# Performance work log

Measured on AMD Instinct MI355X. Metric: run time of the kernel, lower is better.

The kernel has to match this reference:

```python
import jax, jax.numpy as jnp
import numpy as np

B, N, C = 2, 8192, 64      # batch, points, feature channels
M = 2048                    # FPS-sampled centers (num_point)
KS = (16, 32)               # KNN sizes per scale
H, O = 128, 128             # EGNN hidden / output channels
S = len(KS)


def setup_inputs() -> dict:
    key = jax.random.key(0)
    k = jax.random.split(key, 12)
    sc = 0.05
    return {
        "points_xyz": jax.random.normal(k[0], (B, N, 3), jnp.float32),
        "features":   jax.random.normal(k[1], (B, C, N), jnp.float32),
        # edge MLP phi_e: [h_i, h_j, ||x_i-x_j||^2] -> H -> H
        "we1": jax.random.normal(k[2], (S, 2 * C + 1, H)) * sc,
        "be1": jnp.zeros((S, H)),
        "we2": jax.random.normal(k[3], (S, H, H)) * sc,
        "be2": jnp.zeros((S, H)),
        # coord MLP phi_x: H -> 1
        "wx": jax.random.normal(k[4], (S, H, 1)) * sc,
        "bx": jnp.zeros((S, 1)),
        # node MLP phi_h: [h_i, sum_j m_ij] -> H -> O
        "wh1": jax.random.normal(k[5], (S, C + H, H)) * sc,
        "bh1": jnp.zeros((S, H)),
        "wh2": jax.random.normal(k[6], (S, H, O)) * sc,
        "bh2": jnp.zeros((S, O)),
    }


def fps(xyz, m):
    """D-FPS: farthest point sampling by Euclidean distance. xyz (B,N,3) -> idx (B,m) int32."""
    b, n, _ = xyz.shape
    start = jnp.zeros((b,), jnp.int32)
    mind0 = jnp.full((b, n), 1e10, xyz.dtype)

    def step(carry, _):
        mind, last = carry
        lxyz = jnp.take_along_axis(xyz, last[:, None, None], axis=1)  # (B,1,3)
        d = jnp.sum((xyz - lxyz) ** 2, axis=-1)                       # (B,N)
        mind = jnp.minimum(mind, d)
        nxt = jnp.argmax(mind, axis=1).astype(jnp.int32)
        return (mind, nxt), nxt

    (_, _), rest = jax.lax.scan(step, (mind0, start), None, length=m - 1)
    return jnp.concatenate([start[:, None], rest.T], axis=1)  # (B,m)


def _forward(points_xyz, features, we1, be1, we2, be2, wx, bx, wh1, bh1, wh2, bh2):
    idx = fps(points_xyz, M)                                           # (B,M)
    dsamp_xyz = jnp.take_along_axis(points_xyz, idx[:, :, None], axis=1)   # (B,M,3)
    dsamp_feat = jnp.take_along_axis(features, idx[:, None, :], axis=2)    # (B,C,M)
    h_i = dsamp_feat.transpose(0, 2, 1)                                # (B,M,C)

    # pairwise squared distances centers->all points (B,M,N)
    d2 = (jnp.sum(dsamp_xyz ** 2, -1)[:, :, None]
          + jnp.sum(points_xyz ** 2, -1)[:, None, :]
          - 2.0 * jnp.einsum('bmd,bnd->bmn', dsamp_xyz, points_xyz))

    shifted, feats = [], []
    for i, k in enumerate(KS):
        _, nidx = jax.lax.top_k(-d2, k)                                # (B,M,k) KNN indices
        neigh_xyz = jax.vmap(lambda p, ii: p[ii])(points_xyz, nidx)    # (B,M,k,3)
        neigh_feat = jax.vmap(lambda f, ii: f[:, ii])(features, nidx)  # (B,C,M,k)
        h_j = neigh_feat.transpose(0, 2, 3, 1)                         # (B,M,k,C)

        rel = dsamp_xyz[:, :, None, :] - neigh_xyz                     # (B,M,k,3)
        dist2 = jnp.sum(rel * rel, -1, keepdims=True)                  # (B,M,k,1)

        e_in = jnp.concatenate(
            [jnp.broadcast_to(h_i[:, :, None, :], h_j.shape), h_j, dist2], axis=-1)
        m_ij = jax.nn.silu(e_in @ we1[i] + be1[i])
        m_ij = jax.nn.silu(m_ij @ we2[i] + be2[i])                     # (B,M,k,H)

        coef = m_ij @ wx[i] + bx[i]                                    # (B,M,k,1)
        x_shift = dsamp_xyz + jnp.mean(rel * coef, axis=2)             # (B,M,3)

        agg = jnp.sum(m_ij, axis=2)                                    # (B,M,H)
        h_out = jax.nn.silu(jnp.concatenate([h_i, agg], -1) @ wh1[i] + bh1[i]) @ wh2[i] + bh2[i]

        shifted.append(x_shift)
        feats.append(h_out.transpose(0, 2, 1))                         # (B,O,M)

    return (dsamp_xyz,
            jnp.concatenate(shifted, axis=1),    # (B, S*M, 3)
            jnp.concatenate(feats, axis=1),      # (B, S*O, M)
            idx)


def reference(points_xyz, features, we1, be1, we2, be2, wx, bx, wh1, bh1, wh2, bh2):
    return _forward(points_xyz, features, we1, be1, we2, be2, wx, bx, wh1, bh1, wh2, bh2)
```

## Files before the change

### kernel.cpp

```cpp
#include <hip/hip_runtime.h>
#include <stdint.h>
#include <math.h>

#define NPTS  8192
#define NB    2
#define NC    64
#define MCENT 2048
#define HH    128
#define K2NN  32

#define OUT0_OFF 0
#define OUT1_OFF (NB*MCENT*3)
#define OUT2_OFF (OUT1_OFF + NB*2*MCENT*3)
#define OUT3_OFF (OUT2_OFF + NB*2*HH*MCENT)

__device__ __forceinline__ float silu_f(float v){ return v / (1.0f + expf(-v)); }

template<int CTRL>
__device__ __forceinline__ unsigned dppk(unsigned v){
  return (unsigned)__builtin_amdgcn_update_dpp((int)v, (int)v, CTRL, 0xF, 0xF, false);
}
__device__ __forceinline__ unsigned wave_max_u32_sgpr(unsigned v){
  unsigned s;
  s = dppk<0xB1>(v);  v = v > s ? v : s;
  s = dppk<0x4E>(v);  v = v > s ? v : s;
  s = dppk<0x141>(v); v = v > s ? v : s;
  s = dppk<0x140>(v); v = v > s ? v : s;
  s = dppk<0x142>(v); v = v > s ? v : s;
  s = dppk<0x143>(v); v = v > s ? v : s;
  return (unsigned)__builtin_amdgcn_readlane((int)v, 63);
}
__device__ __forceinline__ unsigned wave_min_u32_sgpr(unsigned v){
  unsigned s;
  s = dppk<0xB1>(v);  v = v < s ? v : s;
  s = dppk<0x4E>(v);  v = v < s ? v : s;
  s = dppk<0x141>(v); v = v < s ? v : s;
  s = dppk<0x140>(v); v = v < s ? v : s;
  s = dppk<0x142>(v); v = v < s ? v : s;
  s = dppk<0x143>(v); v = v < s ? v : s;
  return (unsigned)__builtin_amdgcn_readlane((int)v, 63);
}

__device__ __forceinline__ void bar_lds(){
  asm volatile("s_waitcnt lgkmcnt(0)" ::: "memory");
  __builtin_amdgcn_s_barrier();
  __builtin_amdgcn_sched_barrier(0);
}

__global__ __launch_bounds__(1024, 4) void fps_kernel(const float* __restrict__ xyz,
                                                      float* __restrict__ out,
                                                      int* __restrict__ ws_idx){
#pragma clang fp contract(off)
  __shared__ float xs[NPTS], ys[NPTS], zs[NPTS];
  __shared__ unsigned long long warr[2][16];
  const int b    = blockIdx.x;
  const int tid  = threadIdx.x;
  const int lane = tid & 63, wid = tid >> 6;
  const float* P = xyz + (size_t)b * NPTS * 3;

  float x[8], y[8], z[8], mind[8];
  #pragma unroll
  for (int j = 0; j < 8; ++j){
    const int p = tid*8 + j;
    const float px = P[p*3+0], py = P[p*3+1], pz = P[p*3+2];
    x[j] = px; y[j] = py; z[j] = pz; mind[j] = 1e10f;
    xs[p] = px; ys[p] = py; zs[p] = pz;
  }
  float cx = P[0], cy = P[1], cz = P[2];
  if (tid == 0){
    ws_idx[b*MCENT] = 0;
    out[OUT3_OFF + b*MCENT] = 0.0f;
    out[OUT0_OFF + (size_t)(b*MCENT)*3 + 0] = cx;
    out[OUT0_OFF + (size_t)(b*MCENT)*3 + 1] = cy;
    out[OUT0_OFF + (size_t)(b*MCENT)*3 + 2] = cz;
  }
  __syncthreads();

  for (int t = 1; t < MCENT; ++t){
    float bestv = -1.0f; int bestp = tid*8;
    #pragma unroll
    for (int j = 0; j < 8; ++j){
      const float dx = x[j]-cx, dy = y[j]-cy, dz = z[j]-cz;
      const float d  = (dx*dx + dy*dy) + dz*dz;
      const float mn = fminf(mind[j], d);
      mind[j] = mn;
      if (mn > bestv){ bestv = mn; bestp = tid*8 + j; }
    }
    const unsigned vb = __float_as_uint(bestv);
    const unsigned wv = wave_max_u32_sgpr(vb);
    const unsigned long long bal = __ballot(vb == wv);
    const int wl = __ffsll(bal) - 1;
    const int wp = __builtin_amdgcn_readlane(bestp, wl);
    if (lane == 0)
      warr[t & 1][wid] = ((unsigned long long)wv << 32) | (unsigned)(NPTS-1-wp);
    bar_lds();
    unsigned long long kb = warr[t & 1][0];
    #pragma unroll
    for (int w = 1; w < 16; ++w){
      const unsigned long long k2 = warr[t & 1][w];
      if (k2 > kb) kb = k2;
    }
    const int p = NPTS - 1 - (int)(kb & 0xFFFFFFFFULL);
    cx = xs[p]; cy = ys[p]; cz = zs[p];
    if (tid == 0){
      ws_idx[b*MCENT + t] = p;
      out[OUT3_OFF + b*MCENT + t] = (float)p;
      out[OUT0_OFF + (size_t)(b*MCENT + t)*3 + 0] = cx;
      out[OUT0_OFF + (size_t)(b*MCENT + t)*3 + 1] = cy;
      out[OUT0_OFF + (size_t)(b*MCENT + t)*3 + 2] = cz;
    }
  }
}

__global__ __launch_bounds__(256) void knn_kernel(const float* __restrict__ xyz,
                                                  const float* __restrict__ out,
                                                  int* __restrict__ ws_knn){
#pragma clang fp contract(off)
  __shared__ unsigned d2u[NPTS];
  __shared__ unsigned long long warr[2][4];
  const int blk = blockIdx.x;
  const int b = blk / MCENT, m = blk % MCENT;
  const int tid = threadIdx.x;
  const float* P = xyz + (size_t)b*NPTS*3;
  const float cx = out[OUT0_OFF + (size_t)(b*MCENT+m)*3 + 0];
  const float cy = out[OUT0_OFF + (size_t)(b*MCENT+m)*3 + 1];
  const float cz = out[OUT0_OFF + (size_t)(b*MCENT+m)*3 + 2];
  const float cn = (cx*cx + cy*cy) + cz*cz;

  unsigned long long best = ~0ULL, second = ~0ULL;
  #pragma unroll 4
  for (int j = 0; j < NPTS/256; ++j){
    const int p = tid + 256*j;
    const float px = P[p*3+0], py = P[p*3+1], pz = P[p*3+2];
    const float pn = (px*px + py*py) + pz*pz;
    const float e  = (cx*px + cy*py) + cz*pz;
    const float d2 = (cn + pn) - 2.0f*e;
    unsigned u = __float_as_uint(d2);
    u = (u & 0x80000000u) ? ~u : (u | 0x80000000u);
    d2u[p] = u;
    const unsigned long long kk = ((unsigned long long)u << 32) | (unsigned)p;
    if      (kk < best)  { second = best; best = kk; }
    else if (kk < second){ second = kk; }
  }
  __syncthreads();

  for (int it = 0; it < K2NN; ++it){
    const unsigned vb = (unsigned)(best >> 32);
    const unsigned wv = wave_min_u32_sgpr(vb);
    const unsigned long long bal = __ballot(vb == wv);
    unsigned long long k;
    if (__popcll(bal) == 1){
      const int wl = __ffsll(bal) - 1;
      const unsigned lp = (unsigned)__builtin_amdgcn_readlane((int)(unsigned)best, wl);
      k = ((unsigned long long)wv << 32) | lp;
    } else {
      k = best;
      #pragma unroll
      for (int o = 32; o > 0; o >>= 1){
        const unsigned long long k2 = __shfl_xor(k, o);
        if (k2 < k) k = k2;
      }
    }
    if ((tid & 63) == 0) warr[it & 1][tid >> 6] = k;
    __syncthreads();
    unsigned long long kb = warr[it & 1][0];
    #pragma unroll
    for (int w = 1; w < 4; ++w){
      const unsigned long long k2 = warr[it & 1][w];
      if (k2 < kb) kb = k2;
    }
    const unsigned p = (unsigned)kb;
    if (tid == 0) ws_knn[(size_t)blk*K2NN + it] = (int)p;
    if (best == kb){
      d2u[p] = 0xFFFFFFFFu;
      best = second; second = ~0ULL;
      if (best == ~0ULL){
        #pragma unroll 4
        for (int j = 0; j < NPTS/256; ++j){
          const int q = tid + 256*j;
          const unsigned long long kk = ((unsigned long long)d2u[q] << 32) | (unsigned)q;
          if      (kk < best)  { second = best; best = kk; }
          else if (kk < second){ second = kk; }
        }
      }
    }
  }
}

#define S1STR 132

template<int KNB>
__device__ __forceinline__ void egnn_scale(
    int isc, int b, int m, int tid,
    const float* __restrict__ we1, const float* __restrict__ be1,
    const float* __restrict__ we2, const float* __restrict__ be2,
    const float* __restrict__ wxw, const float* __restrict__ bxw,
    const float* __restrict__ wh1, const float* __restrict__ bh1,
    const float* __restrict__ wh2, const float* __restrict__ bh2,
    const float* hi, const float (*hj)[NC], const float (*rel)[3],
    const float* d2s, float (*s1)[S1STR], float (*s2)[S1STR],
    float* coefs, float* aggs, float* t1,
    float cx, float cy, float cz, float* __restrict__ out)
{
  constexpr int KH = KNB/2;
  const int h  = tid & 127;
  const int jg = tid >> 7;
  const int j0 = jg * KH;
  const float* W1 = we1 + (size_t)isc*129*HH;
  const float* W2 = we2 + (size_t)isc*HH*HH;

  float shi = be1[isc*HH + h];
  for (int r = 0; r < NC; ++r) shi += hi[r] * W1[r*HH + h];
  float acc[KH];
  #pragma unroll
  for (int jl = 0; jl < KH; ++jl) acc[jl] = shi;
  for (int r4 = 0; r4 < NC/4; ++r4){
    const float w0 = W1[(NC + 4*r4+0)*HH + h];
    const float w1 = W1[(NC + 4*r4+1)*HH + h];
    const float w2 = W1[(NC + 4*r4+2)*HH + h];
    const float w3 = W1[(NC + 4*r4+3)*HH + h];
    #pragma unroll
    for (int jl = 0; jl < KH; ++jl){
      const float4 v = *(const float4*)&hj[j0+jl][4*r4];
      acc[jl] += v.x*w0; acc[jl] += v.y*w1; acc[jl] += v.z*w2; acc[jl] += v.w*w3;
    }
  }
  {
    const float wd = W1[128*HH + h];
    #pragma unroll
    for (int jl = 0; jl < KH; ++jl)
      s1[j0+jl][h] = silu_f(acc[jl] + d2s[j0+jl]*wd);
  }
  __syncthreads();

  float acc2[KH];
  {
    const float b2 = be2[isc*HH + h];
    #pragma unroll
    for (int jl = 0; jl < KH; ++jl) acc2[jl] = b2;
  }
  for (int r4 = 0; r4 < HH/4; ++r4){
    const float w0 = W2[(4*r4+0)*HH + h];
    const float w1 = W2[(4*r4+1)*HH + h];
    const float w2 = W2[(4*r4+2)*HH + h];
    const float w3 = W2[(4*r4+3)*HH + h];
    #pragma unroll
    for (int jl = 0; jl < KH; ++jl){
      const float4 v = *(const float4*)&s1[j0+jl][4*r4];
      acc2[jl] += v.x*w0; acc2[jl] += v.y*w1; acc2[jl] += v.z*w2; acc2[jl] += v.w*w3;
    }
  }
  #pragma unroll
  for (int jl = 0; jl < KH; ++jl)
    s2[j0+jl][h] = silu_f(acc2[jl]);
  __syncthreads();

  if (tid < HH){
    float a = 0.f;
    #pragma unroll
    for (int j = 0; j < KNB; ++j) a += s2[j][tid];
    aggs[tid] = a;
  } else if (tid < HH + KNB){
    const int j = tid - HH;
    const float* WX = wxw + isc*HH;
    float c = 0.f;
    for (int r = 0; r < HH; ++r) c += s2[j][r]*WX[r];
    coefs[j] = c + bxw[isc];
  }
  __syncthreads();

  if (tid < 3){
    float s = 0.f;
    #pragma unroll
    for (int j = 0; j < KNB; ++j) s += rel[j][tid]*coefs[j];
    const float cc = (tid==0) ? cx : ((tid==1) ? cy : cz);
    out[OUT1_OFF + ((size_t)(b*2 + isc)*MCENT + m)*3 + tid] = cc + s*(1.0f/KNB);
  }

  if (tid < HH){
    const float* WH1 = wh1 + (size_t)isc*(NC+HH)*HH;
    float n = bh1[isc*HH + tid];
    for (int r = 0; r < NC; ++r) n += hi[r]*WH1[r*HH + tid];
    for (int r = 0; r < HH; ++r) n += aggs[r]*WH1[(NC+r)*HH + tid];
    t1[tid] = silu_f(n);
  }
  __syncthreads();

  if (tid < HH){
    const float* WH2 = wh2 + (size_t)isc*HH*HH;
    float v = bh2[isc*HH + tid];
    for (int r = 0; r < HH; ++r) v += t1[r]*WH2[r*HH + tid];
    out[OUT2_OFF + ((size_t)(b*2*HH) + isc*HH + tid)*MCENT + m] = v;
  }
  __syncthreads();
}

__global__ __launch_bounds__(256) void egnn_kernel(
    const float* __restrict__ xyz,  const float* __restrict__ feat,
    const float* __restrict__ we1,  const float* __restrict__ be1,
    const float* __restrict__ we2,  const float* __restrict__ be2,
    const float* __restrict__ wxw,  const float* __restrict__ bxw,
    const float* __restrict__ wh1,  const float* __restrict__ bh1,
    const float* __restrict__ wh2,  const float* __restrict__ bh2,
    const int* __restrict__ ws_idx, const int* __restrict__ ws_knn,
    float* __restrict__ out)
{
  __shared__ __align__(16) float hi[NC];
  __shared__ __align__(16) float hj[K2NN][NC];
  __shared__ float rel[K2NN][3];
  __shared__ float d2s[K2NN];
  __shared__ __align__(16) float s1[K2NN][S1STR];
  __shared__ __align__(16) float s2[K2NN][S1STR];
  __shared__ float coefs[K2NN];
  __shared__ float aggs[HH];
  __shared__ float t1[HH];
  __shared__ int   nidx[K2NN];

  const int blk = blockIdx.x;
  const int b = blk / MCENT, m = blk % MCENT;
  const int tid = threadIdx.x;
  const float* P = xyz + (size_t)b*NPTS*3;
  const float cx = out[OUT0_OFF + (size_t)(b*MCENT+m)*3 + 0];
  const float cy = out[OUT0_OFF + (size_t)(b*MCENT+m)*3 + 1];
  const float cz = out[OUT0_OFF + (size_t)(b*MCENT+m)*3 + 2];

  const int ci = ws_idx[b*MCENT + m];
  if (tid < NC)   hi[tid]   = feat[((size_t)b*NC + tid)*NPTS + ci];
  if (tid < K2NN) nidx[tid] = ws_knn[(size_t)blk*K2NN + tid];
  __syncthreads();

  if (tid < K2NN){
    const int p = nidx[tid];
    const float rx = cx - P[p*3+0];
    const float ry = cy - P[p*3+1];
    const float rz = cz - P[p*3+2];
    rel[tid][0]=rx; rel[tid][1]=ry; rel[tid][2]=rz;
    d2s[tid] = rx*rx + ry*ry + rz*rz;
  }
  {
    const int j  = tid >> 3;
    const int c0 = (tid & 7) * 8;
    const int p  = nidx[j];
    #pragma unroll
    for (int q = 0; q < 8; ++q)
      hj[j][c0+q] = feat[((size_t)b*NC + c0 + q)*NPTS + p];
  }
  __syncthreads();

  egnn_scale<16>(0, b, m, tid, we1, be1, we2, be2, wxw, bxw, wh1, bh1, wh2, bh2,
                 hi, hj, rel, d2s, s1, s2, coefs, aggs, t1, cx, cy, cz, out);
  egnn_scale<32>(1, b, m, tid, we1, be1, we2, be2, wxw, bxw, wh1, bh1, wh2, bh2,
                 hi, hj, rel, d2s, s1, s2, coefs, aggs, t1, cx, cy, cz, out);
}

extern "C" void kernel_launch(void* const* d_in, const int* in_sizes, int n_in,
                              void* d_out, int out_size, void* d_ws, size_t ws_size,
                              hipStream_t stream){
  const float* xyz = (const float*)d_in[0];
  const float* feat= (const float*)d_in[1];
  const float* we1 = (const float*)d_in[2];
  const float* be1 = (const float*)d_in[3];
  const float* we2 = (const float*)d_in[4];
  const float* be2 = (const float*)d_in[5];
  const float* wxw = (const float*)d_in[6];
  const float* bxw = (const float*)d_in[7];
  const float* wh1 = (const float*)d_in[8];
  const float* bh1 = (const float*)d_in[9];
  const float* wh2 = (const float*)d_in[10];
  const float* bh2 = (const float*)d_in[11];
  float* out = (float*)d_out;

  int* ws_idx = (int*)d_ws;
  int* ws_knn = ws_idx + NB*MCENT;

  fps_kernel <<<dim3(NB),        dim3(1024), 0, stream>>>(xyz, out, ws_idx);
  knn_kernel <<<dim3(NB*MCENT),  dim3(256),  0, stream>>>(xyz, out, ws_knn);
  egnn_kernel<<<dim3(NB*MCENT),  dim3(256),  0, stream>>>(xyz, feat,
      we1, be1, we2, be2, wxw, bxw, wh1, bh1, wh2, bh2, ws_idx, ws_knn, out);
}
```

Before: 2.665 ms.

## Fuse KNN into EGNN kernel and shrink FPS block to 256 threads

The KNN selection moves into the EGNN kernel. Its distance buffer shares one LDS arena with the EGNN scratch arrays, and the neighbour indices stay in shared memory instead of passing through a workspace buffer and a separate launch. FPS now runs 256 threads with 32 points per thread, which cuts the cross-wave reduction to 4 waves per iteration. The aim is to make FPS's serial loop, which dominates runtime, cheaper per step. In exchange each thread has more register pressure and does more serial work per step, and the fused kernel uses more LDS, which may lower occupancy.

```diff
diff --git a/kernel.cpp b/kernel.cpp
--- a/kernel.cpp
+++ b/kernel.cpp
@@ -47,21 +47,21 @@
   __builtin_amdgcn_sched_barrier(0);
 }
 
-__global__ __launch_bounds__(1024, 4) void fps_kernel(const float* __restrict__ xyz,
-                                                      float* __restrict__ out,
-                                                      int* __restrict__ ws_idx){
+__global__ __launch_bounds__(256, 2) void fps_kernel(const float* __restrict__ xyz,
+                                                     float* __restrict__ out,
+                                                     int* __restrict__ ws_idx){
 #pragma clang fp contract(off)
   __shared__ float xs[NPTS], ys[NPTS], zs[NPTS];
-  __shared__ unsigned long long warr[2][16];
+  __shared__ unsigned long long warr[2][4];
   const int b    = blockIdx.x;
   const int tid  = threadIdx.x;
   const int lane = tid & 63, wid = tid >> 6;
   const float* P = xyz + (size_t)b * NPTS * 3;
 
-  float x[8], y[8], z[8], mind[8];
+  float x[32], y[32], z[32], mind[32];
   #pragma unroll
-  for (int j = 0; j < 8; ++j){
-    const int p = tid*8 + j;
+  for (int j = 0; j < 32; ++j){
+    const int p = tid*32 + j;
     const float px = P[p*3+0], py = P[p*3+1], pz = P[p*3+2];
     x[j] = px; y[j] = py; z[j] = pz; mind[j] = 1e10f;
     xs[p] = px; ys[p] = py; zs[p] = pz;
@@ -77,14 +77,14 @@
   __syncthreads();
 
   for (int t = 1; t < MCENT; ++t){
-    float bestv = -1.0f; int bestp = tid*8;
-    #pragma unroll
-    for (int j = 0; j < 8; ++j){
+    float bestv = -1.0f; int bestp = tid*32;
+    #pragma unroll
+    for (int j = 0; j < 32; ++j){
       const float dx = x[j]-cx, dy = y[j]-cy, dz = z[j]-cz;
       const float d  = (dx*dx + dy*dy) + dz*dz;
       const float mn = fminf(mind[j], d);
       mind[j] = mn;
-      if (mn > bestv){ bestv = mn; bestp = tid*8 + j; }
+      if (mn > bestv){ bestv = mn; bestp = tid*32 + j; }
     }
     const unsigned vb = __float_as_uint(bestv);
     const unsigned wv = wave_max_u32_sgpr(vb);
@@ -96,7 +96,7 @@
     bar_lds();
     unsigned long long kb = warr[t & 1][0];
     #pragma unroll
-    for (int w = 1; w < 16; ++w){
+    for (int w = 1; w < 4; ++w){
       const unsigned long long k2 = warr[t & 1][w];
       if (k2 > kb) kb = k2;
     }
@@ -112,82 +112,20 @@
   }
 }
 
-__global__ __launch_bounds__(256) void knn_kernel(const float* __restrict__ xyz,
-                                                  const float* __restrict__ out,
-                                                  int* __restrict__ ws_knn){
-#pragma clang fp contract(off)
-  __shared__ unsigned d2u[NPTS];
-  __shared__ unsigned long long warr[2][4];
-  const int blk = blockIdx.x;
-  const int b = blk / MCENT, m = blk % MCENT;
-  const int tid = threadIdx.x;
-  const float* P = xyz + (size_t)b*NPTS*3;
-  const float cx = out[OUT0_OFF + (size_t)(b*MCENT+m)*3 + 0];
-  const float cy = out[OUT0_OFF + (size_t)(b*MCENT+m)*3 + 1];
-  const float cz = out[OUT0_OFF + (size_t)(b*MCENT+m)*3 + 2];
-  const float cn = (cx*cx + cy*cy) + cz*cz;
-
-  unsigned long long best = ~0ULL, second = ~0ULL;
-  #pragma unroll 4
-  for (int j = 0; j < NPTS/256; ++j){
-    const int p = tid + 256*j;
-    const float px = P[p*3+0], py = P[p*3+1], pz = P[p*3+2];
-    const float pn = (px*px + py*py) + pz*pz;
-    const float e  = (cx*px + cy*py) + cz*pz;
-    const float d2 = (cn + pn) - 2.0f*e;
-    unsigned u = __float_as_uint(d2);
-    u = (u & 0x80000000u) ? ~u : (u | 0x80000000u);
-    d2u[p] = u;
-    const unsigned long long kk = ((unsigned long long)u << 32) | (unsigned)p;
-    if      (kk < best)  { second = best; best = kk; }
-    else if (kk < second){ second = kk; }
-  }
-  __syncthreads();
-
-  for (int it = 0; it < K2NN; ++it){
-    const unsigned vb = (unsigned)(best >> 32);
-    const unsigned wv = wave_min_u32_sgpr(vb);
-    const unsigned long long bal = __ballot(vb == wv);
-    unsigned long long k;
-    if (__popcll(bal) == 1){
-      const int wl = __ffsll(bal) - 1;
-      const unsigned lp = (unsigned)__builtin_amdgcn_readlane((int)(unsigned)best, wl);
-      k = ((unsigned long long)wv << 32) | lp;
-    } else {
-      k = best;
-      #pragma unroll
-      for (int o = 32; o > 0; o >>= 1){
-        const unsigned long long k2 = __shfl_xor(k, o);
-        if (k2 < k) k = k2;
-      }
-    }
-    if ((tid & 63) == 0) warr[it & 1][tid >> 6] = k;
-    __syncthreads();
-    unsigned long long kb = warr[it & 1][0];
-    #pragma unroll
-    for (int w = 1; w < 4; ++w){
-      const unsigned long long k2 = warr[it & 1][w];
-      if (k2 < kb) kb = k2;
-    }
-    const unsigned p = (unsigned)kb;
-    if (tid == 0) ws_knn[(size_t)blk*K2NN + it] = (int)p;
-    if (best == kb){
-      d2u[p] = 0xFFFFFFFFu;
-      best = second; second = ~0ULL;
-      if (best == ~0ULL){
-        #pragma unroll 4
-        for (int j = 0; j < NPTS/256; ++j){
-          const int q = tid + 256*j;
-          const unsigned long long kk = ((unsigned long long)d2u[q] << 32) | (unsigned)q;
-          if      (kk < best)  { second = best; best = kk; }
-          else if (kk < second){ second = kk; }
-        }
-      }
-    }
-  }
-}
-
 #define S1STR 132
+#define C_D2U   0
+#define C_S1    0
+#define C_S2    16896
+#define C_HJ    33792
+#define C_HI    41984
+#define C_REL   42240
+#define C_D2S   42624
+#define C_AGG   42752
+#define C_T1    43264
+#define C_COEF  43776
+#define C_NIDX  43904
+#define C_WARR  44032
+#define C_SIZE  44096
 
 template<int KNB>
 __device__ __forceinline__ void egnn_scale(
@@ -295,26 +233,29 @@
   __syncthreads();
 }
 
-__global__ __launch_bounds__(256) void egnn_kernel(
+__global__ __launch_bounds__(256) void knn_egnn_kernel(
     const float* __restrict__ xyz,  const float* __restrict__ feat,
     const float* __restrict__ we1,  const float* __restrict__ be1,
     const float* __restrict__ we2,  const float* __restrict__ be2,
     const float* __restrict__ wxw,  const float* __restrict__ bxw,
     const float* __restrict__ wh1,  const float* __restrict__ bh1,
     const float* __restrict__ wh2,  const float* __restrict__ bh2,
-    const int* __restrict__ ws_idx, const int* __restrict__ ws_knn,
-    float* __restrict__ out)
+    const int* __restrict__ ws_idx, float* __restrict__ out)
 {
-  __shared__ __align__(16) float hi[NC];
-  __shared__ __align__(16) float hj[K2NN][NC];
-  __shared__ float rel[K2NN][3];
-  __shared__ float d2s[K2NN];
-  __shared__ __align__(16) float s1[K2NN][S1STR];
-  __shared__ __align__(16) float s2[K2NN][S1STR];
-  __shared__ float coefs[K2NN];
-  __shared__ float aggs[HH];
-  __shared__ float t1[HH];
-  __shared__ int   nidx[K2NN];
+#pragma clang fp contract(off)
+  __shared__ __align__(16) char smem[C_SIZE];
+  unsigned* d2u = (unsigned*)(smem + C_D2U);
+  float (*s1)[S1STR] = (float (*)[S1STR])(smem + C_S1);
+  float (*s2)[S1STR] = (float (*)[S1STR])(smem + C_S2);
+  float (*hj)[NC]    = (float (*)[NC])(smem + C_HJ);
+  float* hi    = (float*)(smem + C_HI);
+  float (*rel)[3] = (float (*)[3])(smem + C_REL);
+  float* d2s   = (float*)(smem + C_D2S);
+  float* aggs  = (float*)(smem + C_AGG);
+  float* t1    = (float*)(smem + C_T1);
+  float* coefs = (float*)(smem + C_COEF);
+  int*   nidx  = (int*)(smem + C_NIDX);
+  unsigned long long (*warr)[4] = (unsigned long long (*)[4])(smem + C_WARR);
 
   const int blk = blockIdx.x;
   const int b = blk / MCENT, m = blk % MCENT;
@@ -324,11 +265,71 @@
   const float cy = out[OUT0_OFF + (size_t)(b*MCENT+m)*3 + 1];
   const float cz = out[OUT0_OFF + (size_t)(b*MCENT+m)*3 + 2];
 
+  {
+    const float cn = (cx*cx + cy*cy) + cz*cz;
+    unsigned long long best = ~0ULL, second = ~0ULL;
+    #pragma unroll 4
+    for (int j = 0; j < NPTS/256; ++j){
+      const int p = tid + 256*j;
+      const float px = P[p*3+0], py = P[p*3+1], pz = P[p*3+2];
+      const float pn = (px*px + py*py) + pz*pz;
+      const float e  = (cx*px + cy*py) + cz*pz;
+      const float d2 = (cn + pn) - 2.0f*e;
+      unsigned u = __float_as_uint(d2);
+      u = (u & 0x80000000u) ? ~u : (u | 0x80000000u);
+      d2u[p] = u;
+      const unsigned long long kk = ((unsigned long long)u << 32) | (unsigned)p;
+      if      (kk < best)  { second = best; best = kk; }
+      else if (kk < second){ second = kk; }
+    }
+    __syncthreads();
+
+    for (int it = 0; it < K2NN; ++it){
+      const unsigned vb = (unsigned)(best >> 32);
+      const unsigned wv = wave_min_u32_sgpr(vb);
+      const unsigned long long bal = __ballot(vb == wv);
+      unsigned long long k;
+      if (__popcll(bal) == 1){
+        const int wl = __ffsll(bal) - 1;
+        const unsigned lp = (unsigned)__builtin_amdgcn_readlane((int)(unsigned)best, wl);
+        k = ((unsigned long long)wv << 32) | lp;
+      } else {
+        k = best;
+        #pragma unroll
+        for (int o = 32; o > 0; o >>= 1){
+          const unsigned long long k2 = __shfl_xor(k, o);
+          if (k2 < k) k = k2;
+        }
+      }
+      if ((tid & 63) == 0) warr[it & 1][tid >> 6] = k;
+      __syncthreads();
+      unsigned long long kb = warr[it & 1][0];
+      #pragma unroll
+      for (int w = 1; w < 4; ++w){
+        const unsigned long long k2 = warr[it & 1][w];
+        if (k2 < kb) kb = k2;
+      }
+      const unsigned p = (unsigned)kb;
+      if (tid == 0) nidx[it] = (int)p;
+      if (best == kb){
+        d2u[p] = 0xFFFFFFFFu;
+        best = second; second = ~0ULL;
+        if (best == ~0ULL){
+          #pragma unroll 4
+          for (int j = 0; j < NPTS/256; ++j){
+            const int q = tid + 256*j;
+            const unsigned long long kk = ((unsigned long long)d2u[q] << 32) | (unsigned)q;
+            if      (kk < best)  { second = best; best = kk; }
+            else if (kk < second){ second = kk; }
+          }
+        }
+      }
+    }
+    __syncthreads();
+  }
+
   const int ci = ws_idx[b*MCENT + m];
-  if (tid < NC)   hi[tid]   = feat[((size_t)b*NC + tid)*NPTS + ci];
-  if (tid < K2NN) nidx[tid] = ws_knn[(size_t)blk*K2NN + tid];
-  __syncthreads();
-
+  if (tid < NC) hi[tid] = feat[((size_t)b*NC + tid)*NPTS + ci];
   if (tid < K2NN){
     const int p = nidx[tid];
     const float rx = cx - P[p*3+0];
@@ -371,10 +372,8 @@
   float* out = (float*)d_out;
 
   int* ws_idx = (int*)d_ws;
-  int* ws_knn = ws_idx + NB*MCENT;
-
-  fps_kernel <<<dim3(NB),        dim3(1024), 0, stream>>>(xyz, out, ws_idx);
-  knn_kernel <<<dim3(NB*MCENT),  dim3(256),  0, stream>>>(xyz, out, ws_knn);
-  egnn_kernel<<<dim3(NB*MCENT),  dim3(256),  0, stream>>>(xyz, feat,
-      we1, be1, we2, be2, wxw, bxw, wh1, bh1, wh2, bh2, ws_idx, ws_knn, out);
-}
+
+  fps_kernel     <<<dim3(NB),       dim3(256), 0, stream>>>(xyz, out, ws_idx);
+  knn_egnn_kernel<<<dim3(NB*MCENT), dim3(256), 0, stream>>>(xyz, feat,
+      we1, be1, we2, be2, wxw, bxw, wh1, bh1, wh2, bh2, ws_idx, out);
+}
```

Result: faster. 2.301 ms (-13.7%).
